# Kernel optimization log

Hardware: AMD Instinct MI355X
Metric: run time of the kernel (lower is better)

## Reference

```python
import jax, jax.numpy as jnp
import numpy as np

B, N, DIM = 4, 2048, 1024
HEADS, DHEAD = 16, 64
INNER = HEADS * DHEAD  # 1024


def _sigma(t):
    # elu(x) + 1 feature map (strictly positive)
    return jax.nn.elu(t) + 1.0


def setup_inputs() -> dict:
    key = jax.random.key(0)
    k1, k2, k3, k4, k5 = jax.random.split(key, 5)
    x = jax.random.normal(k1, (B, N, DIM), dtype=jnp.float32)
    M = jax.random.normal(k2, (B, HEADS, DHEAD, DHEAD), dtype=jnp.float32)
    Z = jnp.ones((B, HEADS, DHEAD, 1), dtype=jnp.float32)
    W_qkv = jax.random.normal(k3, (DIM, 3 * INNER), dtype=jnp.float32) * (DIM ** -0.5)
    beta_lin = jnp.ones((1,), dtype=jnp.float32) * 4.6     # Linear_Attention.beta
    beta_gate = jax.random.normal(k4, (1, HEADS, 1, 1), dtype=jnp.float32)  # per-head gate
    return {"x": x, "M": M, "Z": Z, "W_qkv": W_qkv, "beta_lin": beta_lin, "beta_gate": beta_gate}


def reference(x, M, Z, W_qkv, beta_lin, beta_gate):
    b, n, _ = x.shape
    scale = DHEAD ** -0.5

    qkv = x @ W_qkv                                   # [b, n, 3*inner]
    q, k, v = jnp.split(qkv, 3, axis=-1)
    # b n (h d) -> b h n d
    to_heads = lambda t: t.reshape(b, n, HEADS, DHEAD).transpose(0, 2, 1, 3)
    q, k, v = to_heads(q), to_heads(k), to_heads(v)

    # ---- linear-attention compressive memory branch ----
    sq = _sigma(q)                                    # [b h n d]
    sk = _sigma(k)
    A_mem = jnp.einsum('bhnd,bhdv->bhnv', sq, M) / jnp.einsum('bhnd,bhdi->bhni', sq, Z)
    moment = jnp.einsum('bhnd,bhdv->bhnv', sk, M) / jnp.einsum('bhnd,bhdi->bhni', sk, Z)

    # EMA state update (training path)
    beta_m = jnp.clip(jax.nn.sigmoid(beta_lin), 0.9, 0.999)  # scalar in (0.9, 0.999)
    Z_new = beta_m * Z + jnp.sum(sk, axis=-2)[..., None]      # [b h d 1]
    M_new = beta_m * M + jnp.einsum('bhnd,bhnv->bhdv', sk, v - moment)

    # ---- standard dot-product attention branch ----
    dots = jnp.einsum('bhid,bhjd->bhij', q, k) * scale
    attn = jax.nn.softmax(dots, axis=-1)
    A_dot = jnp.einsum('bhij,bhjd->bhid', attn, v)

    # ---- learned per-head gate ----
    g = jax.nn.sigmoid(beta_gate)                     # [1 h 1 1]
    A = g * A_mem + (1.0 - g) * A_dot                 # [b h n d]
    A = A.transpose(0, 2, 1, 3).reshape(b, n, INNER)  # b h n d -> b n (h d)
    return (A, M_new, Z_new)
```

## Files before the change

### kernel.cpp

```cpp
#include <hip/hip_runtime.h>
#include <math.h>

#define B_ 4
#define N_ 2048
#define DIM_ 1024
#define H_ 16
#define D_ 64
#define INNER_ 1024
#define BH_ (B_*H_)

#define A_ELEMS  (B_*N_*INNER_)
#define M_ELEMS  (BH_*D_*D_)
#define Z_ELEMS  (BH_*D_)

#define SC_LOG2E 0.18033688011112042f

typedef __attribute__((ext_vector_type(8))) short short8;
typedef __attribute__((ext_vector_type(4))) float f32x4;
typedef __attribute__((ext_vector_type(4))) unsigned short us4;
typedef unsigned short u16;

typedef const unsigned int __attribute__((address_space(1))) gu32;
typedef unsigned int __attribute__((address_space(3))) su32;

__device__ __forceinline__ u16 f2bf(float f) {
    unsigned int u = __float_as_uint(f);
    u += 0x7fffu + ((u >> 16) & 1u);
    return (u16)(u >> 16);
}
__device__ __forceinline__ float bf2f(u16 s) {
    return __uint_as_float(((unsigned int)s) << 16);
}
__device__ __forceinline__ float sigma_f(float x) {
    return x > 0.f ? x + 1.f : __expf(x);
}
__device__ __forceinline__ short8 sig8(short8 in) {
    short8 out;
    u16* ip = (u16*)&in; u16* op = (u16*)&out;
    #pragma unroll
    for (int c = 0; c < 8; c++) op[c] = f2bf(sigma_f(bf2f(ip[c])));
    return out;
}

__global__ __launch_bounds__(256) void prep(
    const float* __restrict__ x,  u16* __restrict__ xb,
    const float* __restrict__ W,  u16* __restrict__ Wt,
    const float* __restrict__ M,  const float* __restrict__ Z,
    const float* __restrict__ beta_lin,
    float* __restrict__ outM, float* __restrict__ outZ) {
    const int bid = blockIdx.x;
    const int t   = threadIdx.x;
    if (bid < 8192) {
        long i = ((long)bid * 256 + t) * 4;
        float4 f = *(const float4*)&x[i];
        us4 o = {f2bf(f.x), f2bf(f.y), f2bf(f.z), f2bf(f.w)};
        *(us4*)&xb[i] = o;
    } else if (bid < 8960) {
        __shared__ u16 T[64 * 68];
        const int b2 = bid - 8192;
        const int n0 = (b2 % 48) * 64, k0 = (b2 / 48) * 64;
        #pragma unroll
        for (int i = 0; i < 4; i++) {
            int r  = (t >> 4) + i * 16;
            int c4 = (t & 15) * 4;
            float4 f = *(const float4*)&W[(long)(k0 + r) * 3072 + n0 + c4];
            T[(c4 + 0) * 68 + r] = f2bf(f.x);
            T[(c4 + 1) * 68 + r] = f2bf(f.y);
            T[(c4 + 2) * 68 + r] = f2bf(f.z);
            T[(c4 + 3) * 68 + r] = f2bf(f.w);
        }
        __syncthreads();
        #pragma unroll
        for (int i = 0; i < 4; i++) {
            int n  = (t >> 4) + i * 16;
            int k4 = (t & 15) * 4;
            us4 o;
            o.x = T[n * 68 + k4];     o.y = T[n * 68 + k4 + 1];
            o.z = T[n * 68 + k4 + 2]; o.w = T[n * 68 + k4 + 3];
            *(us4*)&Wt[(long)(n0 + n) * 1024 + k0 + k4] = o;
        }
    } else {
        float beta = 1.f / (1.f + __expf(-beta_lin[0]));
        beta = fminf(fmaxf(beta, 0.9f), 0.999f);
        int i = (bid - 8960) * 256 + t;
        if (i < M_ELEMS) outM[i] = beta * M[i];
        if (i < Z_ELEMS) outZ[i] = beta * Z[i];
    }
}

__global__ __launch_bounds__(256) void qkv_mfma(
    const u16* __restrict__ xb, const u16* __restrict__ Wt,
    u16* __restrict__ q, u16* __restrict__ k, u16* __restrict__ v) {
    __shared__ u16 As[3][128 * 32];
    __shared__ u16 Bs[3][128 * 32];
    const int t = threadIdx.x, w = t >> 6, lane = t & 63;
    const int quad = lane >> 4, l16 = lane & 15;

    const int lin = blockIdx.x;
    const int wg  = (lin & 7) * 192 + (lin >> 3);
    const int j0  = (wg % 24) * 128;
    const int m0  = (wg / 24) * 128;
    const int mw = (w >> 1) * 64, nw = (w & 1) * 64;

    const int srow = t >> 2;
    const int scol = (t & 3) * 8;

    const u16* pa0 = xb + (long)(m0 + srow) * 1024 + scol;
    const u16* pa1 = pa0 + (long)64 * 1024;
    const u16* pb0 = Wt + (long)(j0 + srow) * 1024 + scol;
    const u16* pb1 = pb0 + (long)64 * 1024;
    su32* da0 = (su32*)&As[0][srow * 32 + scol];
    su32* da1 = (su32*)&As[0][(srow + 64) * 32 + scol];
    su32* db0 = (su32*)&Bs[0][srow * 32 + scol];
    su32* db1 = (su32*)&Bs[0][(srow + 64) * 32 + scol];
    const int half = 128 * 32 / 2;

    f32x4 acc[4][4] = {};

    __builtin_amdgcn_global_load_lds((gu32*)pa0, da0, 16, 0, 0);
    __builtin_amdgcn_global_load_lds((gu32*)pa1, da1, 16, 0, 0);
    __builtin_amdgcn_global_load_lds((gu32*)pb0, db0, 16, 0, 0);
    __builtin_amdgcn_global_load_lds((gu32*)pb1, db1, 16, 0, 0);
    pa0 += 32; pa1 += 32; pb0 += 32; pb1 += 32;
    {
        const int o = half;
        __builtin_amdgcn_global_load_lds((gu32*)pa0, da0 + o, 16, 0, 0);
        __builtin_amdgcn_global_load_lds((gu32*)pa1, da1 + o, 16, 0, 0);
        __builtin_amdgcn_global_load_lds((gu32*)pb0, db0 + o, 16, 0, 0);
        __builtin_amdgcn_global_load_lds((gu32*)pb1, db1 + o, 16, 0, 0);
        pa0 += 32; pa1 += 32; pb0 += 32; pb1 += 32;
    }

    #pragma unroll 1
    for (int kt = 0; kt < 31; ++kt) {
        asm volatile("s_waitcnt vmcnt(4)" ::: "memory");
        __builtin_amdgcn_s_barrier();

        if (kt + 2 < 32) {
            const int o = ((kt + 2) % 3) * half;
            __builtin_amdgcn_global_load_lds((gu32*)pa0, da0 + o, 16, 0, 0);
            __builtin_amdgcn_global_load_lds((gu32*)pa1, da1 + o, 16, 0, 0);
            __builtin_amdgcn_global_load_lds((gu32*)pb0, db0 + o, 16, 0, 0);
            __builtin_amdgcn_global_load_lds((gu32*)pb1, db1 + o, 16, 0, 0);
            pa0 += 32; pa1 += 32; pb0 += 32; pb1 += 32;
        }

        const int cs = (kt % 3) * (128 * 32);
        short8 af[4], bf[4];
        #pragma unroll
        for (int mt = 0; mt < 4; mt++)
            af[mt] = *(const short8*)&As[0][cs + (mw + mt * 16 + l16) * 32 + quad * 8];
        #pragma unroll
        for (int nt = 0; nt < 4; nt++)
            bf[nt] = *(const short8*)&Bs[0][cs + (nw + nt * 16 + l16) * 32 + quad * 8];
        #pragma unroll
        for (int mt = 0; mt < 4; mt++)
            #pragma unroll
            for (int nt = 0; nt < 4; nt++)
                acc[mt][nt] = __builtin_amdgcn_mfma_f32_16x16x32_bf16(
                    af[mt], bf[nt], acc[mt][nt], 0, 0, 0);
    }

    {
        asm volatile("s_waitcnt vmcnt(0)" ::: "memory");
        __builtin_amdgcn_s_barrier();
        const int cs = (31 % 3) * (128 * 32);
        short8 af[4], bf[4];
        #pragma unroll
        for (int mt = 0; mt < 4; mt++)
            af[mt] = *(const short8*)&As[0][cs + (mw + mt * 16 + l16) * 32 + quad * 8];
        #pragma unroll
        for (int nt = 0; nt < 4; nt++)
            bf[nt] = *(const short8*)&Bs[0][cs + (nw + nt * 16 + l16) * 32 + quad * 8];
        #pragma unroll
        for (int mt = 0; mt < 4; mt++)
            #pragma unroll
            for (int nt = 0; nt < 4; nt++)
                acc[mt][nt] = __builtin_amdgcn_mfma_f32_16x16x32_bf16(
                    af[mt], bf[nt], acc[mt][nt], 0, 0, 0);
    }

    const int cb0 = j0 + nw;
    const int which = cb0 >> 10;
    u16* dstsel = (which == 0) ? q : (which == 1) ? k : v;
    const int bq = (m0 + mw) >> 11;
    const int nb = (m0 + mw) & 2047;
    const int lanoff = quad * 256 + l16;
    #pragma unroll
    for (int nt = 0; nt < 4; nt++) {
        const int cb = cb0 + nt * 16;
        const int hh = (cb & 1023) >> 6;
        const int dc = cb & 63;
        u16* dstp = dstsel + ((long)(bq * H_ + hh) * N_ + nb) * D_ + dc;
        #pragma unroll
        for (int mt = 0; mt < 4; mt++)
            #pragma unroll
            for (int r = 0; r < 4; r++)
                dstp[(mt * 16 + r) * 64 + lanoff] = f2bf(acc[mt][nt][r]);
    }
}

__global__ __launch_bounds__(256) void vt_transpose(
    const u16* __restrict__ vb, u16* __restrict__ vT) {
    __shared__ u16 T[64 * 72];
    const int bh = blockIdx.y;
    const int n0 = blockIdx.x * 64;
    const int t  = threadIdx.x;
    const int jj = t >> 3, kg = (t & 7) * 8;
    #pragma unroll
    for (int i = 0; i < 2; i++) {
        int j = jj + i * 32;
        short8 vv = *(const short8*)&vb[(((long)bh * N_ + n0 + j) << 6) + kg];
        u16* vp = (u16*)&vv;
        int jc = j ^ kg;
        #pragma unroll
        for (int c = 0; c < 8; c++) T[(kg + c) * 72 + jc] = vp[c];
    }
    __syncthreads();
    const int d = t >> 2, sg = (t & 3) * 16, xr = d & 56;
    short8 a0 = *(const short8*)&T[d * 72 + (sg ^ xr)];
    short8 a1 = *(const short8*)&T[d * 72 + ((sg + 8) ^ xr)];
    u16* dst = vT + ((long)bh * 64 + d) * 2048 + n0 + sg;
    *(short8*)dst       = a0;
    *(short8*)(dst + 8) = a1;
}

__global__ __launch_bounds__(256) void linear_mfma(
    const u16* __restrict__ qg, const u16* __restrict__ kg_,
    const u16* __restrict__ vTg, const float* __restrict__ Mg,
    const float* __restrict__ Zg, const float* __restrict__ beta_gate,
    float* __restrict__ outA, float* __restrict__ outM, float* __restrict__ outZ) {
    __shared__ u16 MTz[80 * 72];
    __shared__ u16 sqsh[64 * 72];
    __shared__ u16 sksh[64 * 72];
    __shared__ u16 skT[64 * 72];
    __shared__ u16 vmT[80 * 72];
    __shared__ float dks[64];

    const int bh = blockIdx.y, b = bh >> 4, h = bh & 15;
    const int t = threadIdx.x, w = t >> 6, lane = t & 63;
    const int quad = lane >> 4, l16 = lane & 15;
    const long bhN = (long)bh * N_;

    #pragma unroll
    for (int i = 0; i < 4; i++) {
        int d  = (t >> 4) + i * 16;
        int c4 = (t & 15) * 4;
        float4 f = *(const float4*)&Mg[bh * 4096 + d * 64 + c4];
        MTz[(c4 + 0) * 72 + d] = f2bf(f.x);
        MTz[(c4 + 1) * 72 + d] = f2bf(f.y);
        MTz[(c4 + 2) * 72 + d] = f2bf(f.z);
        MTz[(c4 + 3) * 72 + d] = f2bf(f.w);
    }
    if (t < 64) {
        MTz[64 * 72 + t] = f2bf(Zg[bh * 64 + t]);
        vmT[64 * 72 + t] = f2bf(1.0f);
    }
    for (int e = t; e < 15 * 72; e += 256) {
        MTz[65 * 72 + e] = 0;
        vmT[65 * 72 + e] = 0;
    }
    if (t >= 64 && t < 72) { MTz[64 * 72 + t] = 0; vmT[64 * 72 + t] = 0; }

    const float g = 1.f / (1.f + __expf(-beta_gate[h]));

    f32x4 macc[5] = {};

    const int jj = t >> 3;
    const int kgp = (t & 7) * 8;
    const int srow = t >> 2;
    const int sg   = (t & 3) * 16;

    for (int c0 = 0; c0 < 128; c0 += 64) {
        const int n0c = blockIdx.x * 128 + c0;
        __syncthreads();

        #pragma unroll
        for (int i = 0; i < 2; i++) {
            int j = jj + i * 32;
            long gb = ((bhN + n0c + j) << 6) + kgp;
            short8 q8 = sig8(*(const short8*)&qg[gb]);
            short8 k8 = sig8(*(const short8*)&kg_[gb]);
            *(short8*)&sqsh[j * 72 + kgp] = q8;
            *(short8*)&sksh[j * 72 + kgp] = k8;
            u16* kp = (u16*)&k8;
            int jc = j ^ kgp;
            #pragma unroll
            for (int c = 0; c < 8; c++) skT[(kgp + c) * 72 + jc] = kp[c];
        }
        {
            const u16* vp = vTg + ((long)bh * 64 + srow) * 2048 + n0c + sg;
            *(short8*)&vmT[srow * 72 + sg]     = *(const short8*)vp;
            *(short8*)&vmT[srow * 72 + sg + 8] = *(const short8*)(vp + 8);
        }
        __syncthreads();

        {
            short8 a0 = *(const short8*)&sqsh[(w * 16 + l16) * 72 + quad * 8];
            short8 a1 = *(const short8*)&sqsh[(w * 16 + l16) * 72 + 32 + quad * 8];
            f32x4 am[5];
            #pragma unroll
            for (int ct = 0; ct < 5; ct++) {
                short8 b0 = *(const short8*)&MTz[(ct * 16 + l16) * 72 + quad * 8];
                short8 b1 = *(const short8*)&MTz[(ct * 16 + l16) * 72 + 32 + quad * 8];
                f32x4 acc = {};
                acc = __builtin_amdgcn_mfma_f32_16x16x32_bf16(a0, b0, acc, 0, 0, 0);
                acc = __builtin_amdgcn_mfma_f32_16x16x32_bf16(a1, b1, acc, 0, 0, 0);
                am[ct] = acc;
            }
            #pragma unroll
            for (int r = 0; r < 4; r++) {
                float dq  = __shfl(am[4][r], lane & 48, 64);
                float inv = __builtin_amdgcn_rcpf(dq);
                int n = n0c + w * 16 + quad * 4 + r;
                long row = ((long)(b * N_ + n)) * INNER_ + h * 64;
                #pragma unroll
                for (int ct = 0; ct < 4; ct++)
                    outA[row + ct * 16 + l16] = g * am[ct][r] * inv;
            }
        }

        f32x4 mt_[4];
        {
            short8 a0 = *(const short8*)&MTz[(w * 16 + l16) * 72 + quad * 8];
            short8 a1 = *(const short8*)&MTz[(w * 16 + l16) * 72 + 32 + quad * 8];
            #pragma unroll
            for (int ct = 0; ct < 4; ct++) {
                short8 b0 = *(const short8*)&sksh[(ct * 16 + l16) * 72 + quad * 8];
                short8 b1 = *(const short8*)&sksh[(ct * 16 + l16) * 72 + 32 + quad * 8];
                f32x4 acc = {};
                acc = __builtin_amdgcn_mfma_f32_16x16x32_bf16(a0, b0, acc, 0, 0, 0);
                acc = __builtin_amdgcn_mfma_f32_16x16x32_bf16(a1, b1, acc, 0, 0, 0);
                mt_[ct] = acc;
            }
            short8 z0 = *(const short8*)&MTz[(64 + l16) * 72 + quad * 8];
            short8 z1 = *(const short8*)&MTz[(64 + l16) * 72 + 32 + quad * 8];
            short8 b0 = *(const short8*)&sksh[(w * 16 + l16) * 72 + quad * 8];
            short8 b1 = *(const short8*)&sksh[(w * 16 + l16) * 72 + 32 + quad * 8];
            f32x4 acc = {};
            acc = __builtin_amdgcn_mfma_f32_16x16x32_bf16(z0, b0, acc, 0, 0, 0);
            acc = __builtin_amdgcn_mfma_f32_16x16x32_bf16(z1, b1, acc, 0, 0, 0);
            if (quad == 0) dks[w * 16 + l16] = __builtin_amdgcn_rcpf(acc[0]);
        }
        __syncthreads();

        #pragma unroll
        for (int ct = 0; ct < 4; ct++) {
            float invdk = dks[ct * 16 + l16];
            #pragma unroll
            for (int r = 0; r < 4; r++) {
                int vd = w * 16 + quad * 4 + r;
                float vv = bf2f(vmT[vd * 72 + ct * 16 + l16]);
                vmT[vd * 72 + ct * 16 + l16] = f2bf(vv - mt_[ct][r] * invdk);
            }
        }
        __syncthreads();

        {
            int drow = w * 16 + l16, xr = drow & 56;
            short8 a0 = *(const short8*)&skT[drow * 72 + ((quad * 8) ^ xr)];
            short8 a1 = *(const short8*)&skT[drow * 72 + ((32 + quad * 8) ^ xr)];
            #pragma unroll
            for (int ct = 0; ct < 5; ct++) {
                short8 b0 = *(const short8*)&vmT[(ct * 16 + l16) * 72 + quad * 8];
                short8 b1 = *(const short8*)&vmT[(ct * 16 + l16) * 72 + 32 + quad * 8];
                macc[ct] = __builtin_amdgcn_mfma_f32_16x16x32_bf16(a0, b0, macc[ct], 0, 0, 0);
                macc[ct] = __builtin_amdgcn_mfma_f32_16x16x32_bf16(a1, b1, macc[ct], 0, 0, 0);
            }
        }
    }

    #pragma unroll
    for (int ct = 0; ct < 4; ct++)
        #pragma unroll
        for (int r = 0; r < 4; r++) {
            int d = w * 16 + quad * 4 + r;
            atomicAdd(&outM[bh * 4096 + d * 64 + ct * 16 + l16], macc[ct][r]);
        }
    if (l16 == 0)
        #pragma unroll
        for (int r = 0; r < 4; r++)
            atomicAdd(&outZ[bh * 64 + w * 16 + quad * 4 + r], macc[4][r]);
}

__global__ __launch_bounds__(256, 2) void flash_mfma(
    const u16* __restrict__ qb, const u16* __restrict__ kb,
    const u16* __restrict__ vTg, const float* __restrict__ beta_gate,
    float* __restrict__ outA) {
    __shared__ u16 Ks[64 * 68];
    __shared__ u16 Vt[64 * 68];

    const int lin = blockIdx.x;
    const int wg  = (lin & 7) * 64 + (lin >> 3);
    const int bh  = wg >> 3;
    const int n0  = (wg & 7) * 256;
    const int b = bh >> 4, h = bh & 15;
    const int t = threadIdx.x, w = t >> 6, lane = t & 63;
    const int quad = lane >> 4, l16 = lane & 15;
    const long bhN = (long)bh * N_;

    const int srow = t >> 2;
    const int sg   = (t & 3) * 16;
    const int jloc = srow & 31;
    const int krow = (srow & 32) + ((jloc & 4) << 2) + ((jloc >> 3) << 2) + (jloc & 3);

    const u16* kbase  = kb + (bhN << 6);
    const u16* vtbase = vTg + (long)bh * 64 * 2048;

    short8 qf[4][2];
    #pragma unroll
    for (int mi = 0; mi < 4; mi++) {
        long qrow = bhN + n0 + w * 64 + mi * 16 + l16;
        qf[mi][0] = *(const short8*)&qb[(qrow << 6) + quad * 8];
        qf[mi][1] = *(const short8*)&qb[(qrow << 6) + 32 + quad * 8];
        #pragma unroll
        for (int z = 0; z < 2; z++) {
            u16* p = (u16*)&qf[mi][z];
            #pragma unroll
            for (int c = 0; c < 8; c++) p[c] = f2bf(bf2f(p[c]) * SC_LOG2E);
        }
    }

    const short8 onesf = {0x3F80, 0x3F80, 0x3F80, 0x3F80,
                          0x3F80, 0x3F80, 0x3F80, 0x3F80};

    short8 kr0, kr1, vr0, vr1;
    {
        const u16* kp = kbase + ((long)srow << 6) + sg;
        kr0 = *(const short8*)kp;
        kr1 = *(const short8*)(kp + 8);
        const u16* vp = vtbase + (long)srow * 2048 + sg;
        vr0 = *(const short8*)vp;
        vr1 = *(const short8*)(vp + 8);
    }

    f32x4 of[4][4] = {};
    f32x4 ol[4] = {};

    for (int j0 = 0; j0 < N_; j0 += 64) {
        __syncthreads();
        *(short8*)&Ks[krow * 68 + sg]     = kr0;
        *(short8*)&Ks[krow * 68 + sg + 8] = kr1;
        *(short8*)&Vt[srow * 68 + sg]     = vr0;
        *(short8*)&Vt[srow * 68 + sg + 8] = vr1;
        __syncthreads();

        if (j0 + 64 < N_) {
            const u16* kp = kbase + ((long)(j0 + 64 + srow) << 6) + sg;
            kr0 = *(const short8*)kp;
            kr1 = *(const short8*)(kp + 8);
            const u16* vp = vtbase + (long)srow * 2048 + j0 + 64 + sg;
            vr0 = *(const short8*)vp;
            vr1 = *(const short8*)(vp + 8);
        }

        #pragma unroll
        for (int g = 0; g < 2; g++) {
            const int rb = g * 32;
            short8 kA0 = *(const short8*)&Ks[(rb + l16) * 68 + quad * 8];
            short8 kA1 = *(const short8*)&Ks[(rb + l16) * 68 + 32 + quad * 8];
            short8 kB0 = *(const short8*)&Ks[(rb + 16 + l16) * 68 + quad * 8];
            short8 kB1 = *(const short8*)&Ks[(rb + 16 + l16) * 68 + 32 + quad * 8];
            short8 vf[4];
            #pragma unroll
            for (int nt = 0; nt < 4; nt++)
                vf[nt] = *(const short8*)&Vt[(nt * 16 + l16) * 68 + rb + quad * 8];

            #pragma unroll
            for (int mi = 0; mi < 4; mi++) {
                f32x4 st0 = {}, st1 = {};
                __builtin_amdgcn_s_setprio(1);
                st0 = __builtin_amdgcn_mfma_f32_16x16x32_bf16(kA0, qf[mi][0], st0, 0, 0, 0);
                st0 = __builtin_amdgcn_mfma_f32_16x16x32_bf16(kA1, qf[mi][1], st0, 0, 0, 0);
                st1 = __builtin_amdgcn_mfma_f32_16x16x32_bf16(kB0, qf[mi][0], st1, 0, 0, 0);
                st1 = __builtin_amdgcn_mfma_f32_16x16x32_bf16(kB1, qf[mi][1], st1, 0, 0, 0);
                __builtin_amdgcn_s_setprio(0);
                float p0 = __builtin_amdgcn_exp2f(st0[0]);
                float p1 = __builtin_amdgcn_exp2f(st0[1]);
                float p2 = __builtin_amdgcn_exp2f(st0[2]);
                float p3 = __builtin_amdgcn_exp2f(st0[3]);
                float p4 = __builtin_amdgcn_exp2f(st1[0]);
                float p5 = __builtin_amdgcn_exp2f(st1[1]);
                float p6 = __builtin_amdgcn_exp2f(st1[2]);
                float p7 = __builtin_amdgcn_exp2f(st1[3]);
                short8 af;
                unsigned int* au = (unsigned int*)&af;
                au[0] = __builtin_amdgcn_perm(__float_as_uint(p1), __float_as_uint(p0),
                                              0x07060302u);
                au[1] = __builtin_amdgcn_perm(__float_as_uint(p3), __float_as_uint(p2),
                                              0x07060302u);
                au[2] = __builtin_amdgcn_perm(__float_as_uint(p5), __float_as_uint(p4),
                                              0x07060302u);
                au[3] = __builtin_amdgcn_perm(__float_as_uint(p7), __float_as_uint(p6),
                                              0x07060302u);
                __builtin_amdgcn_s_setprio(1);
                ol[mi] = __builtin_amdgcn_mfma_f32_16x16x32_bf16(af, onesf, ol[mi], 0, 0, 0);
                #pragma unroll
                for (int nt = 0; nt < 4; nt++)
                    of[mi][nt] = __builtin_amdgcn_mfma_f32_16x16x32_bf16(
                        af, vf[nt], of[mi][nt], 0, 0, 0);
                __builtin_amdgcn_s_setprio(0);
            }
        }
    }

    const float g  = 1.f / (1.f + __expf(-beta_gate[h]));
    const float gi = 1.f - g;
    #pragma unroll
    for (int mi = 0; mi < 4; mi++) {
        #pragma unroll
        for (int r = 0; r < 4; r++) {
            float sc = gi / ol[mi][r];
            int n = n0 + w * 64 + mi * 16 + quad * 4 + r;
            #pragma unroll
            for (int nt = 0; nt < 4; nt++) {
                long idx = ((long)(b * N_ + n)) * INNER_ + h * 64 + nt * 16 + l16;
                outA[idx] += sc * of[mi][nt][r];
            }
        }
    }
}

extern "C" void kernel_launch(void* const* d_in, const int* in_sizes, int n_in,
                              void* d_out, int out_size, void* d_ws, size_t ws_size,
                              hipStream_t stream) {
    const float* x         = (const float*)d_in[0];
    const float* M         = (const float*)d_in[1];
    const float* Z         = (const float*)d_in[2];
    const float* W         = (const float*)d_in[3];
    const float* beta_lin  = (const float*)d_in[4];
    const float* beta_gate = (const float*)d_in[5];

    float* out  = (float*)d_out;
    float* outA = out;
    float* outM = out + A_ELEMS;
    float* outZ = out + A_ELEMS + M_ELEMS;

    u16* xb = (u16*)d_ws;
    u16* Wt = xb + (size_t)8192 * 1024;
    u16* qb = Wt + (size_t)3072 * 1024;
    u16* kb = qb + (size_t)BH_ * N_ * D_;
    u16* vb = kb + (size_t)BH_ * N_ * D_;
    u16* vt = vb + (size_t)BH_ * N_ * D_;

    prep<<<dim3(9984), 256, 0, stream>>>(x, xb, W, Wt, M, Z, beta_lin, outM, outZ);
    qkv_mfma<<<dim3(1536), 256, 0, stream>>>(xb, Wt, qb, kb, vb);
    vt_transpose<<<dim3(N_ / 64, BH_), 256, 0, stream>>>(vb, vt);
    linear_mfma<<<dim3(16, BH_), 256, 0, stream>>>(qb, kb, vt, M, Z, beta_gate,
                                                   outA, outM, outZ);
    flash_mfma<<<dim3(N_ / 256 * BH_), 256, 0, stream>>>(qb, kb, vt, beta_gate, outA);
}
```

Before: 266.4 us.

## Fuse V transpose into QKV GEMM epilogue and enlarge linear-attention chunks

The QKV GEMM now writes V directly in transposed layout by staging each warp's tile through the reused A/B shared buffers. This removes the separate vt_transpose kernel and the intermediate V buffer round-trip. The linear-attention kernel now handles 256 rows per block instead of 128, halving its grid, and uses a separate vT shared buffer so vmT is not overwritten when loaded. Risks are a slower GEMM epilogue for V tiles and lower occupancy or parallelism in the linear kernel.

```diff
diff --git a/kernel.cpp b/kernel.cpp
--- a/kernel.cpp
+++ b/kernel.cpp
@@ -90,7 +90,7 @@
 
 __global__ __launch_bounds__(256) void qkv_mfma(
     const u16* __restrict__ xb, const u16* __restrict__ Wt,
-    u16* __restrict__ q, u16* __restrict__ k, u16* __restrict__ v) {
+    u16* __restrict__ q, u16* __restrict__ k, u16* __restrict__ vt) {
     __shared__ u16 As[3][128 * 32];
     __shared__ u16 Bs[3][128 * 32];
     const int t = threadIdx.x, w = t >> 6, lane = t & 63;
@@ -182,47 +182,44 @@
 
     const int cb0 = j0 + nw;
     const int which = cb0 >> 10;
-    u16* dstsel = (which == 0) ? q : (which == 1) ? k : v;
     const int bq = (m0 + mw) >> 11;
     const int nb = (m0 + mw) & 2047;
-    const int lanoff = quad * 256 + l16;
-    #pragma unroll
-    for (int nt = 0; nt < 4; nt++) {
-        const int cb = cb0 + nt * 16;
-        const int hh = (cb & 1023) >> 6;
-        const int dc = cb & 63;
-        u16* dstp = dstsel + ((long)(bq * H_ + hh) * N_ + nb) * D_ + dc;
-        #pragma unroll
-        for (int mt = 0; mt < 4; mt++)
-            #pragma unroll
-            for (int r = 0; r < 4; r++)
-                dstp[(mt * 16 + r) * 64 + lanoff] = f2bf(acc[mt][nt][r]);
-    }
-}
-
-__global__ __launch_bounds__(256) void vt_transpose(
-    const u16* __restrict__ vb, u16* __restrict__ vT) {
-    __shared__ u16 T[64 * 72];
-    const int bh = blockIdx.y;
-    const int n0 = blockIdx.x * 64;
-    const int t  = threadIdx.x;
-    const int jj = t >> 3, kg = (t & 7) * 8;
-    #pragma unroll
-    for (int i = 0; i < 2; i++) {
-        int j = jj + i * 32;
-        short8 vv = *(const short8*)&vb[(((long)bh * N_ + n0 + j) << 6) + kg];
-        u16* vp = (u16*)&vv;
-        int jc = j ^ kg;
-        #pragma unroll
-        for (int c = 0; c < 8; c++) T[(kg + c) * 72 + jc] = vp[c];
-    }
-    __syncthreads();
-    const int d = t >> 2, sg = (t & 3) * 16, xr = d & 56;
-    short8 a0 = *(const short8*)&T[d * 72 + (sg ^ xr)];
-    short8 a1 = *(const short8*)&T[d * 72 + ((sg + 8) ^ xr)];
-    u16* dst = vT + ((long)bh * 64 + d) * 2048 + n0 + sg;
-    *(short8*)dst       = a0;
-    *(short8*)(dst + 8) = a1;
+    if (which == 2) {
+        const int hh = (cb0 & 1023) >> 6;
+        const int bh = bq * H_ + hh;
+        u16* tb = (w < 2) ? ((u16*)As + w * 4352) : ((u16*)Bs + (w - 2) * 4352);
+        __syncthreads();
+        #pragma unroll
+        for (int nt = 0; nt < 4; nt++)
+            #pragma unroll
+            for (int mt = 0; mt < 4; mt++)
+                #pragma unroll
+                for (int r = 0; r < 4; r++)
+                    tb[(nt * 16 + l16) * 68 + mt * 16 + quad * 4 + r] =
+                        f2bf(acc[mt][nt][r]);
+        u16* dstp = vt + (long)bh * 64 * 2048 + nb;
+        const int nc = (lane & 7) * 8;
+        #pragma unroll
+        for (int i = 0; i < 8; i++) {
+            int dr = (lane >> 3) + i * 8;
+            *(short8*)&dstp[(long)dr * 2048 + nc] = *(const short8*)&tb[dr * 68 + nc];
+        }
+    } else {
+        u16* dstsel = (which == 0) ? q : k;
+        const int lanoff = quad * 256 + l16;
+        #pragma unroll
+        for (int nt = 0; nt < 4; nt++) {
+            const int cb = cb0 + nt * 16;
+            const int hh = (cb & 1023) >> 6;
+            const int dc = cb & 63;
+            u16* dstp = dstsel + ((long)(bq * H_ + hh) * N_ + nb) * D_ + dc;
+            #pragma unroll
+            for (int mt = 0; mt < 4; mt++)
+                #pragma unroll
+                for (int r = 0; r < 4; r++)
+                    dstp[(mt * 16 + r) * 64 + lanoff] = f2bf(acc[mt][nt][r]);
+        }
+    }
 }
 
 __global__ __launch_bounds__(256) void linear_mfma(
@@ -234,6 +231,7 @@
     __shared__ u16 sqsh[64 * 72];
     __shared__ u16 sksh[64 * 72];
     __shared__ u16 skT[64 * 72];
+    __shared__ u16 vT[64 * 72];
     __shared__ u16 vmT[80 * 72];
     __shared__ float dks[64];
 
@@ -271,8 +269,8 @@
     const int srow = t >> 2;
     const int sg   = (t & 3) * 16;
 
-    for (int c0 = 0; c0 < 128; c0 += 64) {
-        const int n0c = blockIdx.x * 128 + c0;
+    for (int c0 = 0; c0 < 256; c0 += 64) {
+        const int n0c = blockIdx.x * 256 + c0;
         __syncthreads();
 
         #pragma unroll
@@ -290,8 +288,8 @@
         }
         {
             const u16* vp = vTg + ((long)bh * 64 + srow) * 2048 + n0c + sg;
-            *(short8*)&vmT[srow * 72 + sg]     = *(const short8*)vp;
-            *(short8*)&vmT[srow * 72 + sg + 8] = *(const short8*)(vp + 8);
+            *(short8*)&vT[srow * 72 + sg]     = *(const short8*)vp;
+            *(short8*)&vT[srow * 72 + sg + 8] = *(const short8*)(vp + 8);
         }
         __syncthreads();
 
@@ -350,7 +348,7 @@
             #pragma unroll
             for (int r = 0; r < 4; r++) {
                 int vd = w * 16 + quad * 4 + r;
-                float vv = bf2f(vmT[vd * 72 + ct * 16 + l16]);
+                float vv = bf2f(vT[vd * 72 + ct * 16 + l16]);
                 vmT[vd * 72 + ct * 16 + l16] = f2bf(vv - mt_[ct][r] * invdk);
             }
         }
@@ -540,13 +538,11 @@
     u16* Wt = xb + (size_t)8192 * 1024;
     u16* qb = Wt + (size_t)3072 * 1024;
     u16* kb = qb + (size_t)BH_ * N_ * D_;
-    u16* vb = kb + (size_t)BH_ * N_ * D_;
-    u16* vt = vb + (size_t)BH_ * N_ * D_;
+    u16* vt = kb + (size_t)BH_ * N_ * D_;
 
     prep<<<dim3(9984), 256, 0, stream>>>(x, xb, W, Wt, M, Z, beta_lin, outM, outZ);
-    qkv_mfma<<<dim3(1536), 256, 0, stream>>>(xb, Wt, qb, kb, vb);
-    vt_transpose<<<dim3(N_ / 64, BH_), 256, 0, stream>>>(vb, vt);
-    linear_mfma<<<dim3(16, BH_), 256, 0, stream>>>(qb, kb, vt, M, Z, beta_gate,
-                                                   outA, outM, outZ);
+    qkv_mfma<<<dim3(1536), 256, 0, stream>>>(xb, Wt, qb, kb, vt);
+    linear_mfma<<<dim3(8, BH_), 256, 0, stream>>>(qb, kb, vt, M, Z, beta_gate,
+                                                  outA, outM, outZ);
     flash_mfma<<<dim3(N_ / 256 * BH_), 256, 0, stream>>>(qb, kb, vt, beta_gate, outA);
 }
```

Result: no change. 267.9 us (+0.6%).

## Fuse linear-attention output into flash kernel epilogue, drop outA read-modify-write

Applied to the files above, without the earlier changes.

The A_mem computation (sigma(q)·M / sigma(q)·Z) moves from linear_mfma into the flash_mfma epilogue. Each output element is now written once with the gated sum of both branches, which removes the global read-modify-write of outA (about 32 MB written then read and rewritten). linear_mfma keeps only the M/Z state update, now covers 256 rows per block, and is launched after flash. The cost is extra shared memory (MTz) and MFMA work in the flash kernel, which is declared with 2 blocks per SM and may lose occupancy.

```diff
diff --git a/kernel.cpp b/kernel.cpp
--- a/kernel.cpp
+++ b/kernel.cpp
@@ -226,18 +226,17 @@
 }
 
 __global__ __launch_bounds__(256) void linear_mfma(
-    const u16* __restrict__ qg, const u16* __restrict__ kg_,
-    const u16* __restrict__ vTg, const float* __restrict__ Mg,
-    const float* __restrict__ Zg, const float* __restrict__ beta_gate,
-    float* __restrict__ outA, float* __restrict__ outM, float* __restrict__ outZ) {
+    const u16* __restrict__ kg_, const u16* __restrict__ vTg,
+    const float* __restrict__ Mg, const float* __restrict__ Zg,
+    float* __restrict__ outM, float* __restrict__ outZ) {
     __shared__ u16 MTz[80 * 72];
-    __shared__ u16 sqsh[64 * 72];
     __shared__ u16 sksh[64 * 72];
     __shared__ u16 skT[64 * 72];
+    __shared__ u16 vT[64 * 72];
     __shared__ u16 vmT[80 * 72];
     __shared__ float dks[64];
 
-    const int bh = blockIdx.y, b = bh >> 4, h = bh & 15;
+    const int bh = blockIdx.y;
     const int t = threadIdx.x, w = t >> 6, lane = t & 63;
     const int quad = lane >> 4, l16 = lane & 15;
     const long bhN = (long)bh * N_;
@@ -262,8 +261,6 @@
     }
     if (t >= 64 && t < 72) { MTz[64 * 72 + t] = 0; vmT[64 * 72 + t] = 0; }
 
-    const float g = 1.f / (1.f + __expf(-beta_gate[h]));
-
     f32x4 macc[5] = {};
 
     const int jj = t >> 3;
@@ -271,17 +268,15 @@
     const int srow = t >> 2;
     const int sg   = (t & 3) * 16;
 
-    for (int c0 = 0; c0 < 128; c0 += 64) {
-        const int n0c = blockIdx.x * 128 + c0;
+    for (int c0 = 0; c0 < 256; c0 += 64) {
+        const int n0c = blockIdx.x * 256 + c0;
         __syncthreads();
 
         #pragma unroll
         for (int i = 0; i < 2; i++) {
             int j = jj + i * 32;
             long gb = ((bhN + n0c + j) << 6) + kgp;
-            short8 q8 = sig8(*(const short8*)&qg[gb]);
             short8 k8 = sig8(*(const short8*)&kg_[gb]);
-            *(short8*)&sqsh[j * 72 + kgp] = q8;
             *(short8*)&sksh[j * 72 + kgp] = k8;
             u16* kp = (u16*)&k8;
             int jc = j ^ kgp;
@@ -290,35 +285,10 @@
         }
         {
             const u16* vp = vTg + ((long)bh * 64 + srow) * 2048 + n0c + sg;
-            *(short8*)&vmT[srow * 72 + sg]     = *(const short8*)vp;
-            *(short8*)&vmT[srow * 72 + sg + 8] = *(const short8*)(vp + 8);
-        }
-        __syncthreads();
-
-        {
-            short8 a0 = *(const short8*)&sqsh[(w * 16 + l16) * 72 + quad * 8];
-            short8 a1 = *(const short8*)&sqsh[(w * 16 + l16) * 72 + 32 + quad * 8];
-            f32x4 am[5];
-            #pragma unroll
-            for (int ct = 0; ct < 5; ct++) {
-                short8 b0 = *(const short8*)&MTz[(ct * 16 + l16) * 72 + quad * 8];
-                short8 b1 = *(const short8*)&MTz[(ct * 16 + l16) * 72 + 32 + quad * 8];
-                f32x4 acc = {};
-                acc = __builtin_amdgcn_mfma_f32_16x16x32_bf16(a0, b0, acc, 0, 0, 0);
-                acc = __builtin_amdgcn_mfma_f32_16x16x32_bf16(a1, b1, acc, 0, 0, 0);
-                am[ct] = acc;
-            }
-            #pragma unroll
-            for (int r = 0; r < 4; r++) {
-                float dq  = __shfl(am[4][r], lane & 48, 64);
-                float inv = __builtin_amdgcn_rcpf(dq);
-                int n = n0c + w * 16 + quad * 4 + r;
-                long row = ((long)(b * N_ + n)) * INNER_ + h * 64;
-                #pragma unroll
-                for (int ct = 0; ct < 4; ct++)
-                    outA[row + ct * 16 + l16] = g * am[ct][r] * inv;
-            }
-        }
+            *(short8*)&vT[srow * 72 + sg]     = *(const short8*)vp;
+            *(short8*)&vT[srow * 72 + sg + 8] = *(const short8*)(vp + 8);
+        }
+        __syncthreads();
 
         f32x4 mt_[4];
         {
@@ -350,7 +320,7 @@
             #pragma unroll
             for (int r = 0; r < 4; r++) {
                 int vd = w * 16 + quad * 4 + r;
-                float vv = bf2f(vmT[vd * 72 + ct * 16 + l16]);
+                float vv = bf2f(vT[vd * 72 + ct * 16 + l16]);
                 vmT[vd * 72 + ct * 16 + l16] = f2bf(vv - mt_[ct][r] * invdk);
             }
         }
@@ -385,10 +355,12 @@
 
 __global__ __launch_bounds__(256, 2) void flash_mfma(
     const u16* __restrict__ qb, const u16* __restrict__ kb,
-    const u16* __restrict__ vTg, const float* __restrict__ beta_gate,
+    const u16* __restrict__ vTg, const float* __restrict__ Mg,
+    const float* __restrict__ Zg, const float* __restrict__ beta_gate,
     float* __restrict__ outA) {
     __shared__ u16 Ks[64 * 68];
     __shared__ u16 Vt[64 * 68];
+    __shared__ u16 MTz[80 * 72];
 
     const int lin = blockIdx.x;
     const int wg  = (lin & 7) * 64 + (lin >> 3);
@@ -504,19 +476,50 @@
         }
     }
 
+    #pragma unroll
+    for (int i = 0; i < 4; i++) {
+        int d  = (t >> 4) + i * 16;
+        int c4 = (t & 15) * 4;
+        float4 f = *(const float4*)&Mg[bh * 4096 + d * 64 + c4];
+        MTz[(c4 + 0) * 72 + d] = f2bf(f.x);
+        MTz[(c4 + 1) * 72 + d] = f2bf(f.y);
+        MTz[(c4 + 2) * 72 + d] = f2bf(f.z);
+        MTz[(c4 + 3) * 72 + d] = f2bf(f.w);
+    }
+    if (t < 64) MTz[64 * 72 + t] = f2bf(Zg[bh * 64 + t]);
+    for (int e = t; e < 15 * 72; e += 256) MTz[65 * 72 + e] = 0;
+    if (t >= 64 && t < 72) MTz[64 * 72 + t] = 0;
+    __syncthreads();
+
     const float g  = 1.f / (1.f + __expf(-beta_gate[h]));
     const float gi = 1.f - g;
-    #pragma unroll
+
+    #pragma unroll 1
     for (int mi = 0; mi < 4; mi++) {
+        long qrow = bhN + n0 + w * 64 + mi * 16 + l16;
+        short8 s0 = sig8(*(const short8*)&qb[(qrow << 6) + quad * 8]);
+        short8 s1 = sig8(*(const short8*)&qb[(qrow << 6) + 32 + quad * 8]);
+        f32x4 am[5];
+        #pragma unroll
+        for (int ct = 0; ct < 5; ct++) {
+            short8 b0 = *(const short8*)&MTz[(ct * 16 + l16) * 72 + quad * 8];
+            short8 b1 = *(const short8*)&MTz[(ct * 16 + l16) * 72 + 32 + quad * 8];
+            f32x4 acc = {};
+            acc = __builtin_amdgcn_mfma_f32_16x16x32_bf16(s0, b0, acc, 0, 0, 0);
+            acc = __builtin_amdgcn_mfma_f32_16x16x32_bf16(s1, b1, acc, 0, 0, 0);
+            am[ct] = acc;
+        }
         #pragma unroll
         for (int r = 0; r < 4; r++) {
-            float sc = gi / ol[mi][r];
+            float dq  = __shfl(am[4][r], lane & 48, 64);
+            float inv = __builtin_amdgcn_rcpf(dq);
+            float scd = gi / ol[mi][r];
             int n = n0 + w * 64 + mi * 16 + quad * 4 + r;
-            #pragma unroll
-            for (int nt = 0; nt < 4; nt++) {
-                long idx = ((long)(b * N_ + n)) * INNER_ + h * 64 + nt * 16 + l16;
-                outA[idx] += sc * of[mi][nt][r];
-            }
+            long row = ((long)(b * N_ + n)) * INNER_ + h * 64;
+            #pragma unroll
+            for (int nt = 0; nt < 4; nt++)
+                outA[row + nt * 16 + l16] =
+                    g * am[nt][r] * inv + scd * of[mi][nt][r];
         }
     }
 }
@@ -546,7 +549,7 @@
     prep<<<dim3(9984), 256, 0, stream>>>(x, xb, W, Wt, M, Z, beta_lin, outM, outZ);
     qkv_mfma<<<dim3(1536), 256, 0, stream>>>(xb, Wt, qb, kb, vb);
     vt_transpose<<<dim3(N_ / 64, BH_), 256, 0, stream>>>(vb, vt);
-    linear_mfma<<<dim3(16, BH_), 256, 0, stream>>>(qb, kb, vt, M, Z, beta_gate,
-                                                   outA, outM, outZ);
-    flash_mfma<<<dim3(N_ / 256 * BH_), 256, 0, stream>>>(qb, kb, vt, beta_gate, outA);
-}
+    flash_mfma<<<dim3(N_ / 256 * BH_), 256, 0, stream>>>(qb, kb, vt, M, Z,
+                                                         beta_gate, outA);
+    linear_mfma<<<dim3(8, BH_), 256, 0, stream>>>(kb, vt, M, Z, outM, outZ);
+}
```

New measurement: 672.4 us. 152% more time.
